# Performance work log

Hardware: AMD Instinct MI355X
Metric: run time of the kernel (lower is better)

## Reference

```python
import jax, jax.numpy as jnp
import numpy as np

N = 8192       # batch size
BIT = 32       # hash code length
NCLASS = 100   # number of classes
ALPHA = 0.1    # config['alpha'] (quantization weight)
BEITA = 1.0    # config['beita'] (classification weight)
GAMMA = 0.1    # config['gamma'] (balancing weight)
P = 2          # config['p']


def setup_inputs() -> dict:
    key = jax.random.key(0)
    k1, k2, k3 = jax.random.split(key, 3)
    u = jax.random.normal(k1, (N, BIT), dtype=jnp.float32)
    Y = jax.random.normal(k2, (N, NCLASS), dtype=jnp.float32)
    labels = jax.random.randint(k3, (N,), 0, NCLASS)
    y = jax.nn.one_hot(labels, NCLASS, dtype=jnp.float32)  # one-hot targets
    return {"u": u, "Y": Y, "y": y}


def _hash_loss(u, y):
    n = u.shape[0]
    theta = (u @ u.T) * 0.5                       # [N, N]
    sim = (y @ y.T > 0).astype(u.dtype)           # [N, N] pairwise same-class
    # log(1 + exp(theta)) - Sim * theta  (logaddexp = stable same math)
    pair = jnp.logaddexp(0.0, theta) - sim * theta
    mask_pos = sim > 0
    s1 = sim.sum() - n                            # positives minus diagonal
    s0 = n * n - sim.sum()                        # negatives
    s0 = jnp.where(s0 == 0, 1.0, s0)
    s1 = jnp.where(s1 == 0, 1.0, s1)
    s = s0 + s1
    scale = jnp.where(mask_pos, s / s1, s / s0)
    pair = pair * scale
    # original subtracts diag of the *detached* rescaled matrix
    pair = pair - jax.lax.stop_gradient(jnp.diag(jnp.diag(pair)))
    count = n * (n - 1) / 2
    return pair.sum() / 2.0 / count


def reference(u, Y, y):
    likelihood_loss = _hash_loss(u, y)
    # CrossEntropyLoss with soft (one-hot float) targets
    logp = jax.nn.log_softmax(Y, axis=-1)
    classification_loss = -(y * logp).sum(axis=-1).mean()
    m = u.mean(axis=1)
    if P == 1:
        quantization_loss = ALPHA * jnp.abs(m).mean()
    else:
        quantization_loss = ALPHA * (m ** 2).mean()
    b = jnp.sign(u)
    balancing_loss = GAMMA * ((u - b) ** 2).mean()
    return likelihood_loss + BEITA * classification_loss + quantization_loss + balancing_loss
```

## Files before the change

kernel.cpp:

```cpp
#include <hip/hip_runtime.h>
#include <math.h>
#include <type_traits>

#define N 8192
#define BIT 32
#define NCLASS 100
#define ALPHA 0.1
#define BEITA 1.0
#define GAMMA 0.1

#define BT 128
#define NT (N / BT)
#define NPAIRBLK (NT * (NT + 1) / 2)
#define NPW (NPAIRBLK * 4)
#define NPREP (N / 8)

#define SCALE_BF 0.84932181f
#define LN2 0.6931471805599453

typedef __attribute__((ext_vector_type(8))) short s16x8;
typedef __attribute__((ext_vector_type(4))) float f32x4;

#if __has_builtin(__builtin_amdgcn_exp2f)
static __device__ __forceinline__ float fexp2(float x) { return __builtin_amdgcn_exp2f(x); }
#else
static __device__ __forceinline__ float fexp2(float x) { return exp2f(x); }
#endif
#if __has_builtin(__builtin_amdgcn_logf)
static __device__ __forceinline__ float flog2(float x) { return __builtin_amdgcn_logf(x); }
#else
static __device__ __forceinline__ float flog2(float x) { return __log2f(x); }
#endif

static __device__ __forceinline__ unsigned short f2bf(float f) {
    unsigned int x = __float_as_uint(f);
    x += 0x7fff + ((x >> 16) & 1);
    return (unsigned short)(x >> 16);
}


__global__ __launch_bounds__(256) void prep_kernel(
    const float* __restrict__ u, const float* __restrict__ Y, const float* __restrict__ y,
    unsigned char* __restrict__ lab8, unsigned short* __restrict__ ubf,
    double* __restrict__ Pc, double* __restrict__ Pm, double* __restrict__ Pb)
{
    const int t = threadIdx.x;
    const int lane = t & 63;
    const int w = t >> 6;
    const int row0 = blockIdx.x * 8;

    float wcls = 0.f;
    #pragma unroll
    for (int rr = 0; rr < 2; ++rr) {
        const int r = row0 + w * 2 + rr;
        const float* Yp = Y + (size_t)r * NCLASS;
        const float* yp = y + (size_t)r * NCLASS;
        const bool has2 = lane < (NCLASS - 64);
        float Y0 = Yp[lane];
        float Y1 = has2 ? Yp[64 + lane] : -1e30f;
        float y0 = yp[lane];
        float y1 = has2 ? yp[64 + lane] : 0.f;
        float m = fmaxf(Y0, Y1);
        #pragma unroll
        for (int o = 32; o; o >>= 1) m = fmaxf(m, __shfl_xor(m, o, 64));
        float e  = __expf(Y0 - m) + (has2 ? __expf(Y1 - m) : 0.f);
        float tg = y0 * Y0 + (has2 ? y1 * Y1 : 0.f);
        #pragma unroll
        for (int o = 32; o; o >>= 1) { e += __shfl_xor(e, o, 64); tg += __shfl_xor(tg, o, 64); }
        unsigned long long b0 = __ballot(y0 > 0.5f);
        unsigned long long b1 = __ballot(has2 && (y1 > 0.5f));
        if (lane == 0) {
            int lbl = b0 ? (__ffsll((long long)b0) - 1) : (64 + __ffsll((long long)b1) - 1);
            lab8[r] = (unsigned char)lbl;
            wcls += m + __logf(e) - tg;
        }
    }

    const size_t uidx = (size_t)row0 * BIT + t;
    const float x = u[uidx];
    ubf[uidx] = f2bf(x * SCALE_BF);
    float bb = (x > 0.f) ? 1.f : ((x < 0.f) ? -1.f : 0.f);
    float d = x - bb;
    float bal = d * d;
    float rs = x;
    #pragma unroll
    for (int o = 1; o < 32; o <<= 1) rs += __shfl_xor(rs, o, 64);
    float mrow = rs * (1.f / BIT);
    float m2 = ((t & 31) == 0) ? mrow * mrow : 0.f;
    #pragma unroll
    for (int o = 32; o; o >>= 1) { m2 += __shfl_down(m2, o, 64); bal += __shfl_down(bal, o, 64); }

    __shared__ double red[4][3];
    if (lane == 0) { red[w][0] = (double)wcls; red[w][1] = (double)m2; red[w][2] = (double)bal; }
    __syncthreads();
    if (t == 0) {
        Pc[blockIdx.x] = red[0][0] + red[1][0] + red[2][0] + red[3][0];
        Pm[blockIdx.x] = red[0][1] + red[1][1] + red[2][1] + red[3][1];
        Pb[blockIdx.x] = red[0][2] + red[1][2] + red[2][2] + red[3][2];
    }
}

__global__ __launch_bounds__(256, 4) void pair_kernel(
    const unsigned short* __restrict__ ubf, const unsigned char* __restrict__ lab8,
    double* __restrict__ Ppos, double* __restrict__ Pneg)
{
    const int b = blockIdx.x;
    int ti = (int)(((float)(2 * NT + 1) - sqrtf((float)((2 * NT + 1) * (2 * NT + 1) - 8 * b))) * 0.5f);
    int S = ti * (2 * NT - ti + 1) / 2;
    if (S > b) { --ti; S = ti * (2 * NT - ti + 1) / 2; }
    else { int S2 = (ti + 1) * (2 * NT - ti) / 2; if (S2 <= b) { ++ti; S = S2; } }
    const int tj = ti + (b - S);
    const int i0 = ti * BT, j0 = tj * BT;

    const int t = threadIdx.x;
    const int lane = t & 63;
    const int w = t >> 6;
    const int wy = w >> 1, wx = w & 1;
    const int quad = lane >> 4, lr = lane & 15;
    const int ar = i0 + wy * 64;
    const int br = j0 + wx * 64;

    s16x8 av[4], bv[4];
    #pragma unroll
    for (int x = 0; x < 4; ++x) {
        av[x] = *(const s16x8*)(ubf + (size_t)(ar + x * 16 + lr) * BIT + quad * 8);
        bv[x] = *(const s16x8*)(ubf + (size_t)(br + x * 16 + lr) * BIT + quad * 8);
    }
    int lavp[4], lbv[4];
    #pragma unroll
    for (int a = 0; a < 4; ++a) lavp[a] = *(const int*)(lab8 + ar + a * 16 + quad * 4);
    #pragma unroll
    for (int c = 0; c < 4; ++c) lbv[c] = (int)lab8[br + c * 16 + lr];

    f32x4 acc[4][4];
    #pragma unroll
    for (int a = 0; a < 4; ++a)
        #pragma unroll
        for (int c = 0; c < 4; ++c)
            acc[a][c] = __builtin_amdgcn_mfma_f32_16x16x32_bf16(
                av[a], bv[c], (f32x4){0.f, 0.f, 0.f, 0.f}, 0, 0, 0);

    float vsum0 = 0.f, vsum1 = 0.f, vsim0 = 0.f, vsim1 = 0.f;
    auto run = [&](auto DIAGC) {
        constexpr bool DIAG = decltype(DIAGC)::value;
        #pragma unroll
        for (int a = 0; a < 4; ++a) {
            #pragma unroll
            for (int r = 0; r < 4; ++r) {
                const int la = (lavp[a] >> (r * 8)) & 0xff;
                const int rowv = a * 16 + quad * 4 + r;
                #pragma unroll
                for (int c = 0; c < 4; ++c) {
                    const float tv = acc[a][c][r];
                    const bool sim = (la == lbv[c]);
                    float x = sim ? -tv : tv;
                    float v = flog2(1.f + fexp2(x));
                    if (DIAG) {
                        const bool keep = (c * 16 + lr) > rowv;
                        v = keep ? v : 0.f;
                    }
                    float vs = sim ? v : 0.f;
                    if (r & 1) { vsum1 += v; vsim1 += vs; }
                    else       { vsum0 += v; vsim0 += vs; }
                }
            }
        }
    };
    if (ti == tj) run(std::integral_constant<bool, true>{});
    else          run(std::integral_constant<bool, false>{});

    float vsum = vsum0 + vsum1, vsim = vsim0 + vsim1;
    #pragma unroll
    for (int o = 32; o; o >>= 1) { vsum += __shfl_down(vsum, o, 64); vsim += __shfl_down(vsim, o, 64); }
    if (lane == 0) {
        Ppos[4 * b + w] = (double)vsim;
        Pneg[4 * b + w] = (double)(vsum - vsim);
    }
}

__global__ __launch_bounds__(256) void fin_kernel(
    const unsigned char* __restrict__ lab8, const double* __restrict__ Ppos,
    const double* __restrict__ Pneg, const double* __restrict__ Pc,
    const double* __restrict__ Pm, const double* __restrict__ Pb, float* __restrict__ out)
{
    __shared__ int h[128];
    __shared__ double red[4][5];
    __shared__ double scd[2];
    const int t = threadIdx.x;
    const int lane = t & 63;
    const int w = t >> 6;

    if (t < 128) h[t] = 0;
    __syncthreads();
    #pragma unroll
    for (int k = 0; k < 32; ++k) atomicAdd(&h[lab8[t + k * 256]], 1);
    __syncthreads();

    if (w == 0) {
        long long c0 = (lane < NCLASS) ? h[lane] : 0;
        long long c1 = (lane + 64 < NCLASS) ? h[lane + 64] : 0;
        long long ss = c0 * c0 + c1 * c1;
        #pragma unroll
        for (int o = 32; o; o >>= 1) ss += __shfl_xor(ss, o, 64);
        if (lane == 0) {
            double s1 = (double)ss - (double)N;
            double s0 = (double)N * (double)N - (double)ss;
            if (s0 == 0.0) s0 = 1.0;
            if (s1 == 0.0) s1 = 1.0;
            double s = s0 + s1;
            scd[0] = (s / s1) * LN2;
            scd[1] = (s / s0) * LN2;
        }
    }

    double p0 = 0, p1 = 0, cc = 0, mm = 0, bb = 0;
    for (int i = t; i < NPW; i += 256)   { p0 += Ppos[i]; p1 += Pneg[i]; }
    for (int i = t; i < NPREP; i += 256) { cc += Pc[i]; mm += Pm[i]; bb += Pb[i]; }
    #pragma unroll
    for (int o = 32; o; o >>= 1) {
        p0 += __shfl_down(p0, o, 64); p1 += __shfl_down(p1, o, 64);
        cc += __shfl_down(cc, o, 64); mm += __shfl_down(mm, o, 64);
        bb += __shfl_down(bb, o, 64);
    }
    if (lane == 0) { red[w][0] = p0; red[w][1] = p1; red[w][2] = cc; red[w][3] = mm; red[w][4] = bb; }
    __syncthreads();
    if (t == 0) {
        double a_pos = red[0][0] + red[1][0] + red[2][0] + red[3][0];
        double a_neg = red[0][1] + red[1][1] + red[2][1] + red[3][1];
        double a_cls = red[0][2] + red[1][2] + red[2][2] + red[3][2];
        double a_m2  = red[0][3] + red[1][3] + red[2][3] + red[3][3];
        double a_bal = red[0][4] + red[1][4] + red[2][4] + red[3][4];
        double pairsum = scd[0] * a_pos + scd[1] * a_neg;
        double lik   = 2.0 * pairsum / ((double)N * (double)(N - 1));
        double cls   = a_cls / (double)N;
        double quant = ALPHA * (a_m2 / (double)N);
        double bal   = GAMMA * (a_bal / ((double)N * (double)BIT));
        out[0] = (float)(lik + BEITA * cls + quant + bal);
    }
}

extern "C" void kernel_launch(void* const* d_in, const int* in_sizes, int n_in,
                              void* d_out, int out_size, void* d_ws, size_t ws_size,
                              hipStream_t stream) {
    const float* u = (const float*)d_in[0];
    const float* Y = (const float*)d_in[1];
    const float* y = (const float*)d_in[2];
    float* out = (float*)d_out;

    char* ws = (char*)d_ws;
    unsigned char*  lab8 = (unsigned char*)(ws + 1024);
    unsigned short* ubf  = (unsigned short*)(ws + 16384);
    double* Ppos = (double*)(ws + 557056);
    double* Pneg = (double*)(ws + 630784);
    double* Pc   = (double*)(ws + 704512);
    double* Pm   = (double*)(ws + 712704);
    double* Pb   = (double*)(ws + 720896);

    prep_kernel<<<NPREP, 256, 0, stream>>>(u, Y, y, lab8, ubf, Pc, Pm, Pb);
    pair_kernel<<<NPAIRBLK, 256, 0, stream>>>(ubf, lab8, Ppos, Pneg);
    fin_kernel<<<1, 256, 0, stream>>>(lab8, Ppos, Pneg, Pc, Pm, Pb, out);
}
```

Before: 93.83 us.

## Process up to three tile pairs per block with prefetched loads

The pair kernel now launches a fixed grid of 694 blocks. Each block handles up to three triangular tile pairs with a stride of that grid size, and loads the next tiles' bf16 rows and labels before running the current tile's MFMA and softplus epilogue, so memory latency overlaps compute. The compile-time diagonal specialization is replaced by a runtime offd mask in the epilogue. Holding several tiles' operands in registers raises register pressure, which is why launch bounds drop to 3 waves per EU; the runtime mask also adds per-element work.

```diff
diff --git a/kernel.cpp b/kernel.cpp
--- a/kernel.cpp
+++ b/kernel.cpp
@@ -1,6 +1,5 @@
 #include <hip/hip_runtime.h>
 #include <math.h>
-#include <type_traits>
 
 #define N 8192
 #define BIT 32
@@ -12,6 +11,7 @@
 #define BT 128
 #define NT (N / BT)
 #define NPAIRBLK (NT * (NT + 1) / 2)
+#define NBLK 694
 #define NPW (NPAIRBLK * 4)
 #define NPREP (N / 8)
 
@@ -100,81 +100,111 @@
     }
 }
 
-__global__ __launch_bounds__(256, 4) void pair_kernel(
+__global__ __launch_bounds__(256, 3) void pair_kernel(
     const unsigned short* __restrict__ ubf, const unsigned char* __restrict__ lab8,
     double* __restrict__ Ppos, double* __restrict__ Pneg)
 {
-    const int b = blockIdx.x;
-    int ti = (int)(((float)(2 * NT + 1) - sqrtf((float)((2 * NT + 1) * (2 * NT + 1) - 8 * b))) * 0.5f);
-    int S = ti * (2 * NT - ti + 1) / 2;
-    if (S > b) { --ti; S = ti * (2 * NT - ti + 1) / 2; }
-    else { int S2 = (ti + 1) * (2 * NT - ti) / 2; if (S2 <= b) { ++ti; S = S2; } }
-    const int tj = ti + (b - S);
-    const int i0 = ti * BT, j0 = tj * BT;
-
     const int t = threadIdx.x;
     const int lane = t & 63;
     const int w = t >> 6;
     const int wy = w >> 1, wx = w & 1;
     const int quad = lane >> 4, lr = lane & 15;
-    const int ar = i0 + wy * 64;
-    const int br = j0 + wx * 64;
-
-    s16x8 av[4], bv[4];
-    #pragma unroll
-    for (int x = 0; x < 4; ++x) {
-        av[x] = *(const s16x8*)(ubf + (size_t)(ar + x * 16 + lr) * BIT + quad * 8);
-        bv[x] = *(const s16x8*)(ubf + (size_t)(br + x * 16 + lr) * BIT + quad * 8);
-    }
-    int lavp[4], lbv[4];
-    #pragma unroll
-    for (int a = 0; a < 4; ++a) lavp[a] = *(const int*)(lab8 + ar + a * 16 + quad * 4);
-    #pragma unroll
-    for (int c = 0; c < 4; ++c) lbv[c] = (int)lab8[br + c * 16 + lr];
-
-    f32x4 acc[4][4];
-    #pragma unroll
-    for (int a = 0; a < 4; ++a)
-        #pragma unroll
-        for (int c = 0; c < 4; ++c)
-            acc[a][c] = __builtin_amdgcn_mfma_f32_16x16x32_bf16(
-                av[a], bv[c], (f32x4){0.f, 0.f, 0.f, 0.f}, 0, 0, 0);
-
-    float vsum0 = 0.f, vsum1 = 0.f, vsim0 = 0.f, vsim1 = 0.f;
-    auto run = [&](auto DIAGC) {
-        constexpr bool DIAG = decltype(DIAGC)::value;
+    const int laneoff = lr * BIT + quad * 8;
+
+    auto decode = [&](int b, int& i0, int& j0, bool& offd) {
+        int ti = (int)(((float)(2 * NT + 1) - sqrtf((float)((2 * NT + 1) * (2 * NT + 1) - 8 * b))) * 0.5f);
+        int S = ti * (2 * NT - ti + 1) / 2;
+        if (S > b) { --ti; S = ti * (2 * NT - ti + 1) / 2; }
+        else { int S2 = (ti + 1) * (2 * NT - ti) / 2; if (S2 <= b) { ++ti; S = S2; } }
+        const int tj = ti + (b - S);
+        i0 = ti * BT; j0 = tj * BT; offd = (ti != tj);
+    };
+
+    auto loadt = [&](int i0, int j0, s16x8 (&av)[4], s16x8 (&bv)[4],
+                     int (&lavp)[4], int (&lbv)[4]) {
+        const unsigned short* pa = ubf + (size_t)(i0 + wy * 64) * BIT + laneoff;
+        const unsigned short* pb = ubf + (size_t)(j0 + wx * 64) * BIT + laneoff;
+        #pragma unroll
+        for (int x = 0; x < 4; ++x) {
+            av[x] = *(const s16x8*)(pa + x * 16 * BIT);
+            bv[x] = *(const s16x8*)(pb + x * 16 * BIT);
+        }
+        #pragma unroll
+        for (int a = 0; a < 4; ++a) lavp[a] = *(const int*)(lab8 + i0 + wy * 64 + a * 16 + quad * 4);
+        #pragma unroll
+        for (int c = 0; c < 4; ++c) lbv[c] = (int)lab8[j0 + wx * 64 + c * 16 + lr];
+    };
+
+    auto mfmat = [&](const s16x8 (&av)[4], const s16x8 (&bv)[4], f32x4 (&acc)[4][4]) {
+        #pragma unroll
+        for (int a = 0; a < 4; ++a)
+            #pragma unroll
+            for (int c = 0; c < 4; ++c)
+                acc[a][c] = __builtin_amdgcn_mfma_f32_16x16x32_bf16(
+                    av[a], bv[c], (f32x4){0.f, 0.f, 0.f, 0.f}, 0, 0, 0);
+    };
+
+    auto epit = [&](int b, bool offd, const f32x4 (&acc)[4][4],
+                    const int (&lavp)[4], const int (&lbv)[4]) {
+        float vsum0 = 0.f, vsum1 = 0.f, vsim0 = 0.f, vsim1 = 0.f;
         #pragma unroll
         for (int a = 0; a < 4; ++a) {
             #pragma unroll
             for (int r = 0; r < 4; ++r) {
                 const int la = (lavp[a] >> (r * 8)) & 0xff;
-                const int rowv = a * 16 + quad * 4 + r;
+                const int grow = wy * 64 + a * 16 + quad * 4 + r;
                 #pragma unroll
                 for (int c = 0; c < 4; ++c) {
                     const float tv = acc[a][c][r];
                     const bool sim = (la == lbv[c]);
                     float x = sim ? -tv : tv;
                     float v = flog2(1.f + fexp2(x));
-                    if (DIAG) {
-                        const bool keep = (c * 16 + lr) > rowv;
-                        v = keep ? v : 0.f;
-                    }
+                    const bool keep = offd | ((wx * 64 + c * 16 + lr) > grow);
+                    v = keep ? v : 0.f;
                     float vs = sim ? v : 0.f;
                     if (r & 1) { vsum1 += v; vsim1 += vs; }
                     else       { vsum0 += v; vsim0 += vs; }
                 }
             }
         }
-    };
-    if (ti == tj) run(std::integral_constant<bool, true>{});
-    else          run(std::integral_constant<bool, false>{});
-
-    float vsum = vsum0 + vsum1, vsim = vsim0 + vsim1;
-    #pragma unroll
-    for (int o = 32; o; o >>= 1) { vsum += __shfl_down(vsum, o, 64); vsim += __shfl_down(vsim, o, 64); }
-    if (lane == 0) {
-        Ppos[4 * b + w] = (double)vsim;
-        Pneg[4 * b + w] = (double)(vsum - vsim);
+        float vsum = vsum0 + vsum1, vsim = vsim0 + vsim1;
+        #pragma unroll
+        for (int o = 32; o; o >>= 1) { vsum += __shfl_down(vsum, o, 64); vsim += __shfl_down(vsim, o, 64); }
+        if (lane == 0) {
+            Ppos[4 * b + w] = (double)vsim;
+            Pneg[4 * b + w] = (double)(vsum - vsim);
+        }
+    };
+
+    const int b0 = blockIdx.x;
+    const int b1 = b0 + NBLK;
+    const int b2 = b1 + NBLK;
+    const bool has2 = (b2 < NPAIRBLK);
+
+    int i0A, j0A, i0B, j0B, i0C = 0, j0C = 0;
+    bool odA, odB, odC = false;
+    s16x8 avA[4], bvA[4], avB[4], bvB[4], avC[4], bvC[4];
+    int lavpA[4], lbvA[4], lavpB[4], lbvB[4], lavpC[4], lbvC[4];
+
+    decode(b0, i0A, j0A, odA);
+    loadt(i0A, j0A, avA, bvA, lavpA, lbvA);
+    decode(b1, i0B, j0B, odB);
+    loadt(i0B, j0B, avB, bvB, lavpB, lbvB);
+
+    f32x4 acc[4][4];
+    mfmat(avA, bvA, acc);
+    if (has2) {
+        decode(b2, i0C, j0C, odC);
+        loadt(i0C, j0C, avC, bvC, lavpC, lbvC);
+    }
+    epit(b0, odA, acc, lavpA, lbvA);
+
+    mfmat(avB, bvB, acc);
+    epit(b1, odB, acc, lavpB, lbvB);
+
+    if (has2) {
+        mfmat(avC, bvC, acc);
+        epit(b2, odC, acc, lavpC, lbvC);
     }
 }
 
@@ -257,6 +287,6 @@
     double* Pb   = (double*)(ws + 720896);
 
     prep_kernel<<<NPREP, 256, 0, stream>>>(u, Y, y, lab8, ubf, Pc, Pm, Pb);
-    pair_kernel<<<NPAIRBLK, 256, 0, stream>>>(ubf, lab8, Ppos, Pneg);
+    pair_kernel<<<NBLK, 256, 0, stream>>>(ubf, lab8, Ppos, Pneg);
     fin_kernel<<<1, 256, 0, stream>>>(lab8, Ppos, Pneg, Pc, Pm, Pb, out);
 }
```

After: 98.84 us. 5.3% more time.
